# Kernel tuning notes

Measured on AMD Instinct MI355X. Metric: run time of the kernel, lower is better.

The kernel has to match this reference:

```python
import jax, jax.numpy as jnp
import numpy as np

N_NODES = 100000

def _graphconv(x, edge_src, edge_dst, norm_src, norm_dst, W, b):
    # DGL GraphConv with norm='both': D_out^{-1/2} A D_in^{-1/2} X W + b
    h = x * norm_src[:, None]                       # [N, d] src normalization
    msg = jnp.take(h, edge_src, axis=0)             # [E, d] gather
    agg = jax.ops.segment_sum(msg, edge_dst, num_segments=N_NODES)  # [N, d] scatter-add
    h = agg * norm_dst[:, None]                      # dst normalization
    return h @ W + b

def _degree_norms(edge_src, edge_dst):
    ones = jnp.ones(edge_src.shape[0], dtype=jnp.float32)
    deg_out = jax.ops.segment_sum(ones, edge_src, num_segments=N_NODES)
    deg_in = jax.ops.segment_sum(ones, edge_dst, num_segments=N_NODES)
    norm_src = jnp.where(deg_out > 0, jax.lax.rsqrt(jnp.maximum(deg_out, 1.0)), 0.0)
    norm_dst = jnp.where(deg_in > 0, jax.lax.rsqrt(jnp.maximum(deg_in, 1.0)), 0.0)
    return norm_src, norm_dst

def setup_inputs() -> dict:
    key = jax.random.key(0)
    ks = jax.random.split(key, 8)
    E = 1600000
    in_f, h_f, out_f = 128, 128, 64
    x = jax.random.normal(ks[0], (N_NODES, in_f), dtype=jnp.float32)
    edge_src = jax.random.randint(ks[1], (E,), 0, N_NODES, dtype=jnp.int32)
    edge_dst = jax.random.randint(ks[2], (E,), 0, N_NODES, dtype=jnp.int32)
    def glorot(k, shape):
        lim = np.sqrt(6.0 / (shape[0] + shape[1]))
        return jax.random.uniform(k, shape, jnp.float32, -lim, lim)
    W0 = glorot(ks[3], (in_f, h_f)); b0 = jnp.zeros((h_f,), jnp.float32)
    W1 = glorot(ks[4], (h_f, h_f)); b1 = jnp.zeros((h_f,), jnp.float32)
    W2 = glorot(ks[5], (h_f, out_f)); b2 = jnp.zeros((out_f,), jnp.float32)
    return {"x": x, "edge_src": edge_src, "edge_dst": edge_dst,
            "W0": W0, "b0": b0, "W1": W1, "b1": b1, "W2": W2, "b2": b2}

def reference(x, edge_src, edge_dst, W0, b0, W1, b1, W2, b2):
    norm_src, norm_dst = _degree_norms(edge_src, edge_dst)
    outputs = [x]
    h = jax.nn.relu(_graphconv(x, edge_src, edge_dst, norm_src, norm_dst, W0, b0))
    outputs.append(h)
    h = jax.nn.relu(_graphconv(h, edge_src, edge_dst, norm_src, norm_dst, W1, b1))
    outputs.append(h)
    h = _graphconv(h, edge_src, edge_dst, norm_src, norm_dst, W2, b2)
    outputs.append(h)
    return tuple(outputs)
```

## Files before the change

kernel.cpp:

```cpp
#include <hip/hip_runtime.h>

#define NN 100000
#define NE 1600000
#define NB 391
#define RS 32768
#define KR 4
#define RSL 64
#define SLICE 25000

typedef unsigned int uint;
typedef unsigned short ushort;
typedef unsigned char uchar;
typedef __attribute__((ext_vector_type(8))) short short8;
typedef __attribute__((ext_vector_type(4))) float f32x4;

__device__ __forceinline__ ushort f2bf(float f) {
    uint u = __float_as_uint(f);
    return (ushort)((u + 0x7FFFu + ((u >> 16) & 1u)) >> 16);
}

__device__ __forceinline__ void bf8_add(uint4 q, float* acc) {
    acc[0] += __uint_as_float(q.x << 16);
    acc[1] += __uint_as_float(q.x & 0xFFFF0000u);
    acc[2] += __uint_as_float(q.y << 16);
    acc[3] += __uint_as_float(q.y & 0xFFFF0000u);
    acc[4] += __uint_as_float(q.z << 16);
    acc[5] += __uint_as_float(q.z & 0xFFFF0000u);
    acc[6] += __uint_as_float(q.w << 16);
    acc[7] += __uint_as_float(q.w & 0xFFFF0000u);
}


__global__ __launch_bounds__(256)
void k_hist(const int* __restrict__ src, const int* __restrict__ dst,
            uchar* __restrict__ pout, uchar* __restrict__ pin) {
    int k = blockIdx.x >> 6, r = blockIdx.x & 63;
    __shared__ uint ho[RS / 4], hi[RS / 4];
    for (int i = threadIdx.x; i < RS / 4; i += 256) { ho[i] = 0; hi[i] = 0; }
    __syncthreads();
    int base = k * RS;
    int lo = r * SLICE, hiend = lo + SLICE;
    for (int i = lo + threadIdx.x; i < hiend; i += 256) {
        int s = src[i] - base;
        if ((uint)s < RS) atomicAdd(&ho[s >> 2], 1u << (8 * (s & 3)));
        int d = dst[i] - base;
        if ((uint)d < RS) atomicAdd(&hi[d >> 2], 1u << (8 * (d & 3)));
    }
    __syncthreads();
    uint* po = (uint*)(pout + ((size_t)k * RSL + r) * RS);
    uint* pi = (uint*)(pin + ((size_t)k * RSL + r) * RS);
    for (int i = threadIdx.x; i < RS / 4; i += 256) { po[i] = ho[i]; pi[i] = hi[i]; }
}


__global__ __launch_bounds__(256)
void k_red(const uchar* __restrict__ pout, uchar* __restrict__ pin,
           float* __restrict__ ns, float* __restrict__ nd,
           int* __restrict__ csum, int* __restrict__ bsum) {
    __shared__ int sred[256];
    int t = threadIdx.x;
    int n = blockIdx.x * 256 + t;
    int si = 0;
    if (n < NN) {
        int k = n >> 15, j = n & (RS - 1);
        const uchar* po = pout + (size_t)k * RSL * RS + j;
        uchar* pi = pin + (size_t)k * RSL * RS + j;
        int so = 0;
        #pragma unroll
        for (int r = 0; r < RSL; ++r) so += po[(size_t)r * RS];
        #pragma unroll
        for (int r = 0; r < RSL; ++r) {
            uchar c = pi[(size_t)r * RS];
            pi[(size_t)r * RS] = (uchar)si;
            si += c;
        }
        ns[n] = (so > 0) ? rsqrtf((float)so) : 0.f;
        nd[n] = (si > 0) ? rsqrtf((float)si) : 0.f;
        csum[n] = si;
    }
    sred[t] = si;
    __syncthreads();
    for (int off = 128; off > 0; off >>= 1) {
        if (t < off) sred[t] += sred[t + off];
        __syncthreads();
    }
    if (t == 0) bsum[blockIdx.x] = sred[0];
}


__global__ void k_scanb(const int* __restrict__ bsum, int* __restrict__ bsumex,
                        int* __restrict__ rowptr) {
    __shared__ int s[512];
    int t = threadIdx.x;
    int v = (t < NB) ? bsum[t] : 0;
    s[t] = v;
    __syncthreads();
    for (int off = 1; off < 512; off <<= 1) {
        int add = (t >= off) ? s[t - off] : 0;
        __syncthreads();
        s[t] += add;
        __syncthreads();
    }
    if (t < NB) bsumex[t] = s[t] - v;
    if (t == 0) rowptr[NN] = NE;
}

__global__ void k_rowptr(const int* __restrict__ cnt, const int* __restrict__ bsumex,
                         int* __restrict__ rowptr) {
    __shared__ int s[256];
    int t = threadIdx.x;
    int i = blockIdx.x * 256 + t;
    int v = (i < NN) ? cnt[i] : 0;
    s[t] = v;
    __syncthreads();
    for (int off = 1; off < 256; off <<= 1) {
        int add = (t >= off) ? s[t - off] : 0;
        __syncthreads();
        s[t] += add;
        __syncthreads();
    }
    if (i < NN) rowptr[i] = bsumex[blockIdx.x] + s[t] - v;
}


__global__ __launch_bounds__(256)
void k_fill(const int* __restrict__ src, const int* __restrict__ dst,
            const uchar* __restrict__ pin, const int* __restrict__ rowptr,
            int* __restrict__ csrc) {
    int k = blockIdx.x >> 6, r = blockIdx.x & 63;
    __shared__ uint cur[RS / 2];
    const uchar* pi = pin + ((size_t)k * RSL + r) * RS;
    for (int i = threadIdx.x; i < RS / 2; i += 256) {
        uint a = pi[2 * i], b = pi[2 * i + 1];
        cur[i] = a | (b << 16);
    }
    __syncthreads();
    int base = k * RS;
    int lo = r * SLICE, hiend = lo + SLICE;
    for (int i = lo + threadIdx.x; i < hiend; i += 256) {
        int d = dst[i];
        int j = d - base;
        if ((uint)j < RS) {
            uint old = atomicAdd(&cur[j >> 1], 1u << (16 * (j & 1)));
            int p = (old >> (16 * (j & 1))) & 0xFFFF;
            csrc[rowptr[d] + p] = src[i];
        }
    }
}


__global__ void k_wtall(const float* __restrict__ W0, const float* __restrict__ W1,
                        const float* __restrict__ W2, ushort* __restrict__ WT) {
    int i = blockIdx.x * 256 + threadIdx.x;
    if (i < 16384) {
        int n = i >> 7, k = i & 127;
        WT[i] = f2bf(W0[k * 128 + n]);
    } else if (i < 32768) {
        int j = i - 16384; int n = j >> 7, k = j & 127;
        WT[i] = f2bf(W1[k * 128 + n]);
    } else if (i < 40960) {
        int j = i - 32768; int n = j >> 7, k = j & 127;
        WT[i] = f2bf(W2[k * 64 + n]);
    }
}


__global__ void k_xcvt(const float4* __restrict__ x, float4* __restrict__ out,
                       ushort* __restrict__ xb, int n4) {
    int i = blockIdx.x * blockDim.x + threadIdx.x;
    if (i < n4) {
        float4 v = x[i];
        out[i] = v;
        ushort4 b;
        b.x = f2bf(v.x); b.y = f2bf(v.y); b.z = f2bf(v.z); b.w = f2bf(v.w);
        *(ushort4*)(xb + (size_t)i * 4) = b;
    }
}


template<int NT, int N>
__global__ __launch_bounds__(256)
void k_gemm_mfma(const ushort* __restrict__ Ab, const ushort* __restrict__ WT,
                 const float* __restrict__ ns, ushort* __restrict__ Cb) {
    int tid = threadIdx.x;
    int w = tid >> 6;
    int l = tid & 63;
    int li = l & 15;
    int kg = l >> 4;
    short8 bfrag[NT][4];
    #pragma unroll
    for (int n = 0; n < NT; ++n) {
        int col = w * 16 * NT + n * 16 + li;
        #pragma unroll
        for (int kt = 0; kt < 4; ++kt)
            bfrag[n][kt] = *(const short8*)(WT + (size_t)col * 128 + kt * 32 + kg * 8);
    }
    for (int mg = blockIdx.x; mg < NN / 16; mg += gridDim.x) {
        int row = mg * 16 + li;
        short8 afrag[4];
        #pragma unroll
        for (int kt = 0; kt < 4; ++kt)
            afrag[kt] = *(const short8*)(Ab + (size_t)row * 128 + kt * 32 + kg * 8);
        int crow = mg * 16 + kg * 4;
        float4 nsv = *(const float4*)(ns + crow);
        float nsa[4] = {nsv.x, nsv.y, nsv.z, nsv.w};
        #pragma unroll
        for (int n = 0; n < NT; ++n) {
            f32x4 acc = {0.f, 0.f, 0.f, 0.f};
            #pragma unroll
            for (int kt = 0; kt < 4; ++kt)
                acc = __builtin_amdgcn_mfma_f32_16x16x32_bf16(afrag[kt], bfrag[n][kt], acc, 0, 0, 0);
            int ccol = w * 16 * NT + n * 16 + li;
            #pragma unroll
            for (int r = 0; r < 4; ++r)
                Cb[(size_t)(crow + r) * N + ccol] = f2bf(acc[r] * nsa[r]);
        }
    }
}


template<bool RELU>
__global__ __launch_bounds__(256)
void k_agg128(const ushort* __restrict__ Yb, const int* __restrict__ rowptr,
              const int* __restrict__ csrc, const float* __restrict__ nd,
              const float* __restrict__ bias, float* __restrict__ out,
              ushort* __restrict__ outb) {
    int tid = threadIdx.x;
    int grp = tid >> 4;
    int lane = tid & 15;
    int node = blockIdx.x * 16 + grp;
    int beg = rowptr[node], end = rowptr[node + 1];
    float acc[8] = {0.f, 0.f, 0.f, 0.f, 0.f, 0.f, 0.f, 0.f};
    int e = beg;
    for (; e + 7 < end; e += 8) {
        int s0 = csrc[e];     int s1 = csrc[e + 1];
        int s2 = csrc[e + 2]; int s3 = csrc[e + 3];
        int s4 = csrc[e + 4]; int s5 = csrc[e + 5];
        int s6 = csrc[e + 6]; int s7 = csrc[e + 7];
        uint4 q0 = *(const uint4*)(Yb + (size_t)s0 * 128 + lane * 8);
        uint4 q1 = *(const uint4*)(Yb + (size_t)s1 * 128 + lane * 8);
        uint4 q2 = *(const uint4*)(Yb + (size_t)s2 * 128 + lane * 8);
        uint4 q3 = *(const uint4*)(Yb + (size_t)s3 * 128 + lane * 8);
        uint4 q4 = *(const uint4*)(Yb + (size_t)s4 * 128 + lane * 8);
        uint4 q5 = *(const uint4*)(Yb + (size_t)s5 * 128 + lane * 8);
        uint4 q6 = *(const uint4*)(Yb + (size_t)s6 * 128 + lane * 8);
        uint4 q7 = *(const uint4*)(Yb + (size_t)s7 * 128 + lane * 8);
        bf8_add(q0, acc); bf8_add(q1, acc); bf8_add(q2, acc); bf8_add(q3, acc);
        bf8_add(q4, acc); bf8_add(q5, acc); bf8_add(q6, acc); bf8_add(q7, acc);
    }
    for (; e + 3 < end; e += 4) {
        int s0 = csrc[e];     int s1 = csrc[e + 1];
        int s2 = csrc[e + 2]; int s3 = csrc[e + 3];
        uint4 q0 = *(const uint4*)(Yb + (size_t)s0 * 128 + lane * 8);
        uint4 q1 = *(const uint4*)(Yb + (size_t)s1 * 128 + lane * 8);
        uint4 q2 = *(const uint4*)(Yb + (size_t)s2 * 128 + lane * 8);
        uint4 q3 = *(const uint4*)(Yb + (size_t)s3 * 128 + lane * 8);
        bf8_add(q0, acc); bf8_add(q1, acc); bf8_add(q2, acc); bf8_add(q3, acc);
    }
    for (; e < end; ++e) {
        uint4 q = *(const uint4*)(Yb + (size_t)csrc[e] * 128 + lane * 8);
        bf8_add(q, acc);
    }
    float ndv = nd[node];
    float4 b0 = *(const float4*)(bias + lane * 8);
    float4 b1 = *(const float4*)(bias + lane * 8 + 4);
    float o[8];
    o[0] = acc[0] * ndv + b0.x; o[1] = acc[1] * ndv + b0.y;
    o[2] = acc[2] * ndv + b0.z; o[3] = acc[3] * ndv + b0.w;
    o[4] = acc[4] * ndv + b1.x; o[5] = acc[5] * ndv + b1.y;
    o[6] = acc[6] * ndv + b1.z; o[7] = acc[7] * ndv + b1.w;
    if (RELU) {
        #pragma unroll
        for (int i = 0; i < 8; ++i) o[i] = fmaxf(o[i], 0.f);
    }
    *(float4*)(out + (size_t)node * 128 + lane * 8)     = make_float4(o[0], o[1], o[2], o[3]);
    *(float4*)(out + (size_t)node * 128 + lane * 8 + 4) = make_float4(o[4], o[5], o[6], o[7]);
    short8 ob;
    #pragma unroll
    for (int i = 0; i < 8; ++i) ob[i] = (short)f2bf(o[i]);
    *(short8*)(outb + (size_t)node * 128 + lane * 8) = ob;
}

__global__ __launch_bounds__(256)
void k_agg64(const ushort* __restrict__ Yb, const int* __restrict__ rowptr,
             const int* __restrict__ csrc, const float* __restrict__ nd,
             const float* __restrict__ bias, float* __restrict__ out) {
    int tid = threadIdx.x;
    int grp = tid >> 3;
    int lane = tid & 7;
    int node = blockIdx.x * 32 + grp;
    int beg = rowptr[node], end = rowptr[node + 1];
    float acc[8] = {0.f, 0.f, 0.f, 0.f, 0.f, 0.f, 0.f, 0.f};
    int e = beg;
    for (; e + 7 < end; e += 8) {
        int s0 = csrc[e];     int s1 = csrc[e + 1];
        int s2 = csrc[e + 2]; int s3 = csrc[e + 3];
        int s4 = csrc[e + 4]; int s5 = csrc[e + 5];
        int s6 = csrc[e + 6]; int s7 = csrc[e + 7];
        uint4 q0 = *(const uint4*)(Yb + (size_t)s0 * 64 + lane * 8);
        uint4 q1 = *(const uint4*)(Yb + (size_t)s1 * 64 + lane * 8);
        uint4 q2 = *(const uint4*)(Yb + (size_t)s2 * 64 + lane * 8);
        uint4 q3 = *(const uint4*)(Yb + (size_t)s3 * 64 + lane * 8);
        uint4 q4 = *(const uint4*)(Yb + (size_t)s4 * 64 + lane * 8);
        uint4 q5 = *(const uint4*)(Yb + (size_t)s5 * 64 + lane * 8);
        uint4 q6 = *(const uint4*)(Yb + (size_t)s6 * 64 + lane * 8);
        uint4 q7 = *(const uint4*)(Yb + (size_t)s7 * 64 + lane * 8);
        bf8_add(q0, acc); bf8_add(q1, acc); bf8_add(q2, acc); bf8_add(q3, acc);
        bf8_add(q4, acc); bf8_add(q5, acc); bf8_add(q6, acc); bf8_add(q7, acc);
    }
    for (; e + 3 < end; e += 4) {
        int s0 = csrc[e];     int s1 = csrc[e + 1];
        int s2 = csrc[e + 2]; int s3 = csrc[e + 3];
        uint4 q0 = *(const uint4*)(Yb + (size_t)s0 * 64 + lane * 8);
        uint4 q1 = *(const uint4*)(Yb + (size_t)s1 * 64 + lane * 8);
        uint4 q2 = *(const uint4*)(Yb + (size_t)s2 * 64 + lane * 8);
        uint4 q3 = *(const uint4*)(Yb + (size_t)s3 * 64 + lane * 8);
        bf8_add(q0, acc); bf8_add(q1, acc); bf8_add(q2, acc); bf8_add(q3, acc);
    }
    for (; e < end; ++e) {
        uint4 q = *(const uint4*)(Yb + (size_t)csrc[e] * 64 + lane * 8);
        bf8_add(q, acc);
    }
    float ndv = nd[node];
    float4 b0 = *(const float4*)(bias + lane * 8);
    float4 b1 = *(const float4*)(bias + lane * 8 + 4);
    float4 o0, o1;
    o0.x = acc[0] * ndv + b0.x; o0.y = acc[1] * ndv + b0.y;
    o0.z = acc[2] * ndv + b0.z; o0.w = acc[3] * ndv + b0.w;
    o1.x = acc[4] * ndv + b1.x; o1.y = acc[5] * ndv + b1.y;
    o1.z = acc[6] * ndv + b1.z; o1.w = acc[7] * ndv + b1.w;
    *(float4*)(out + (size_t)node * 64 + lane * 8)     = o0;
    *(float4*)(out + (size_t)node * 64 + lane * 8 + 4) = o1;
}


extern "C" void kernel_launch(void* const* d_in, const int* in_sizes, int n_in,
                              void* d_out, int out_size, void* d_ws, size_t ws_size,
                              hipStream_t stream) {
    const float* x  = (const float*)d_in[0];
    const int* esrc = (const int*)d_in[1];
    const int* edst = (const int*)d_in[2];
    const float* W0 = (const float*)d_in[3];
    const float* b0 = (const float*)d_in[4];
    const float* W1 = (const float*)d_in[5];
    const float* b1 = (const float*)d_in[6];
    const float* W2 = (const float*)d_in[7];
    const float* b2 = (const float*)d_in[8];
    float* out = (float*)d_out;

    float* ns      = (float*)d_ws;
    float* nd      = ns + NN;
    int*   csum    = (int*)(nd + NN);
    int*   rowptr  = csum + NN;
    int*   bsum    = rowptr + NN + 8;
    int*   bsumex  = bsum + 512;
    int*   csrc    = bsumex + 512;
    uchar* pout    = (uchar*)(csrc + NE);
    uchar* pin     = pout + (size_t)KR * RSL * RS;
    ushort* WT0    = (ushort*)(pin + (size_t)KR * RSL * RS);
    ushort* WT1    = WT0 + 128 * 128;
    ushort* WT2    = WT1 + 128 * 128;
    ushort* Y2b    = WT2 + 64 * 128;
    ushort* xb     = Y2b + (size_t)NN * 64;
    ushort* h1b    = xb + (size_t)NN * 128;
    ushort* h2b    = h1b + (size_t)NN * 128;

    float* h1 = out + (size_t)NN * 128;
    float* h2 = h1 + (size_t)NN * 128;
    float* h3 = h2 + (size_t)NN * 128;

    ushort* Y0b = (ushort*)h2;
    ushort* Y1b = (ushort*)h3;

    k_hist<<<KR * RSL, 256, 0, stream>>>(esrc, edst, pout, pin);

    k_red<<<NB, 256, 0, stream>>>(pout, pin, ns, nd, csum, bsum);

    k_scanb<<<1, 512, 0, stream>>>(bsum, bsumex, rowptr);
    k_rowptr<<<NB, 256, 0, stream>>>(csum, bsumex, rowptr);

    k_fill<<<KR * RSL, 256, 0, stream>>>(esrc, edst, pin, rowptr, csrc);

    k_wtall<<<160, 256, 0, stream>>>(W0, W1, W2, WT0);

    k_xcvt<<<(NN * 32 + 255) / 256, 256, 0, stream>>>((const float4*)x, (float4*)out,
                                                      xb, NN * 32);

    k_gemm_mfma<2, 128><<<1024, 256, 0, stream>>>(xb, WT0, ns, Y0b);
    k_agg128<true><<<NN / 16, 256, 0, stream>>>(Y0b, rowptr, csrc, nd, b0, h1, h1b);

    k_gemm_mfma<2, 128><<<1024, 256, 0, stream>>>(h1b, WT1, ns, Y1b);
    k_agg128<true><<<NN / 16, 256, 0, stream>>>(Y1b, rowptr, csrc, nd, b1, h2, h2b);

    k_gemm_mfma<1, 64><<<1024, 256, 0, stream>>>(h2b, WT2, ns, Y2b);
    k_agg64<<<NN / 32, 256, 0, stream>>>(Y2b, rowptr, csrc, nd, b2, h3);
}
```

Measured before the change: 436.4 us.

## Fuse x conversion into first GEMM and fuse aggregation with next-layer GEMM

The separate fp32-to-bf16 conversion of x is folded into the first MFMA GEMM, which now reads fp32 x directly, converts it in registers and writes the copied output. Each 128-wide aggregation kernel now stages its bf16 result for 16 nodes in shared memory and immediately runs the next layer's MFMA projection, so the h1b/h2b bf16 intermediates and two GEMM launches disappear. This removes global round trips and launches, at the cost of per-block weight fragment reloads from global/L2 and a block-wide barrier inside the gather kernel.

```diff
diff --git a/kernel.cpp b/kernel.cpp
--- a/kernel.cpp
+++ b/kernel.cpp
@@ -165,32 +165,19 @@
 }
 
 
-__global__ void k_xcvt(const float4* __restrict__ x, float4* __restrict__ out,
-                       ushort* __restrict__ xb, int n4) {
-    int i = blockIdx.x * blockDim.x + threadIdx.x;
-    if (i < n4) {
-        float4 v = x[i];
-        out[i] = v;
-        ushort4 b;
-        b.x = f2bf(v.x); b.y = f2bf(v.y); b.z = f2bf(v.z); b.w = f2bf(v.w);
-        *(ushort4*)(xb + (size_t)i * 4) = b;
-    }
-}
-
-
-template<int NT, int N>
-__global__ __launch_bounds__(256)
-void k_gemm_mfma(const ushort* __restrict__ Ab, const ushort* __restrict__ WT,
-                 const float* __restrict__ ns, ushort* __restrict__ Cb) {
+__global__ __launch_bounds__(256)
+void k_gemm1(const float* __restrict__ A, const ushort* __restrict__ WT,
+             const float* __restrict__ ns, ushort* __restrict__ Cb,
+             float* __restrict__ xout) {
     int tid = threadIdx.x;
     int w = tid >> 6;
     int l = tid & 63;
     int li = l & 15;
     int kg = l >> 4;
-    short8 bfrag[NT][4];
+    short8 bfrag[2][4];
     #pragma unroll
-    for (int n = 0; n < NT; ++n) {
-        int col = w * 16 * NT + n * 16 + li;
+    for (int n = 0; n < 2; ++n) {
+        int col = w * 32 + n * 16 + li;
         #pragma unroll
         for (int kt = 0; kt < 4; ++kt)
             bfrag[n][kt] = *(const short8*)(WT + (size_t)col * 128 + kt * 32 + kg * 8);
@@ -199,36 +186,54 @@
         int row = mg * 16 + li;
         short8 afrag[4];
         #pragma unroll
-        for (int kt = 0; kt < 4; ++kt)
-            afrag[kt] = *(const short8*)(Ab + (size_t)row * 128 + kt * 32 + kg * 8);
+        for (int kt = 0; kt < 4; ++kt) {
+            const float* ap = A + (size_t)row * 128 + kt * 32 + kg * 8;
+            float4 a0 = *(const float4*)ap;
+            float4 a1 = *(const float4*)(ap + 4);
+            if (w == 0) {
+                float* op = xout + (size_t)row * 128 + kt * 32 + kg * 8;
+                *(float4*)op = a0;
+                *(float4*)(op + 4) = a1;
+            }
+            short8 af;
+            af[0] = (short)f2bf(a0.x); af[1] = (short)f2bf(a0.y);
+            af[2] = (short)f2bf(a0.z); af[3] = (short)f2bf(a0.w);
+            af[4] = (short)f2bf(a1.x); af[5] = (short)f2bf(a1.y);
+            af[6] = (short)f2bf(a1.z); af[7] = (short)f2bf(a1.w);
+            afrag[kt] = af;
+        }
         int crow = mg * 16 + kg * 4;
         float4 nsv = *(const float4*)(ns + crow);
         float nsa[4] = {nsv.x, nsv.y, nsv.z, nsv.w};
         #pragma unroll
-        for (int n = 0; n < NT; ++n) {
+        for (int n = 0; n < 2; ++n) {
             f32x4 acc = {0.f, 0.f, 0.f, 0.f};
             #pragma unroll
             for (int kt = 0; kt < 4; ++kt)
                 acc = __builtin_amdgcn_mfma_f32_16x16x32_bf16(afrag[kt], bfrag[n][kt], acc, 0, 0, 0);
-            int ccol = w * 16 * NT + n * 16 + li;
+            int ccol = w * 32 + n * 16 + li;
             #pragma unroll
             for (int r = 0; r < 4; ++r)
-                Cb[(size_t)(crow + r) * N + ccol] = f2bf(acc[r] * nsa[r]);
+                Cb[(size_t)(crow + r) * 128 + ccol] = f2bf(acc[r] * nsa[r]);
         }
     }
 }
 
 
-template<bool RELU>
-__global__ __launch_bounds__(256)
-void k_agg128(const ushort* __restrict__ Yb, const int* __restrict__ rowptr,
-              const int* __restrict__ csrc, const float* __restrict__ nd,
-              const float* __restrict__ bias, float* __restrict__ out,
-              ushort* __restrict__ outb) {
+template<int NOUT>
+__global__ __launch_bounds__(256)
+void k_agg_gemm(const ushort* __restrict__ Yb, const int* __restrict__ rowptr,
+                const int* __restrict__ csrc, const float* __restrict__ nd,
+                const float* __restrict__ bias, const float* __restrict__ ns,
+                const ushort* __restrict__ WT, float* __restrict__ hout,
+                ushort* __restrict__ Yout) {
+    constexpr int NT = NOUT / 64;
+    __shared__ ushort sA[16][136];
     int tid = threadIdx.x;
     int grp = tid >> 4;
     int lane = tid & 15;
-    int node = blockIdx.x * 16 + grp;
+    int node_base = blockIdx.x * 16;
+    int node = node_base + grp;
     int beg = rowptr[node], end = rowptr[node + 1];
     float acc[8] = {0.f, 0.f, 0.f, 0.f, 0.f, 0.f, 0.f, 0.f};
     int e = beg;
@@ -265,20 +270,43 @@
     float4 b0 = *(const float4*)(bias + lane * 8);
     float4 b1 = *(const float4*)(bias + lane * 8 + 4);
     float o[8];
-    o[0] = acc[0] * ndv + b0.x; o[1] = acc[1] * ndv + b0.y;
-    o[2] = acc[2] * ndv + b0.z; o[3] = acc[3] * ndv + b0.w;
-    o[4] = acc[4] * ndv + b1.x; o[5] = acc[5] * ndv + b1.y;
-    o[6] = acc[6] * ndv + b1.z; o[7] = acc[7] * ndv + b1.w;
-    if (RELU) {
-        #pragma unroll
-        for (int i = 0; i < 8; ++i) o[i] = fmaxf(o[i], 0.f);
-    }
-    *(float4*)(out + (size_t)node * 128 + lane * 8)     = make_float4(o[0], o[1], o[2], o[3]);
-    *(float4*)(out + (size_t)node * 128 + lane * 8 + 4) = make_float4(o[4], o[5], o[6], o[7]);
+    o[0] = fmaxf(acc[0] * ndv + b0.x, 0.f); o[1] = fmaxf(acc[1] * ndv + b0.y, 0.f);
+    o[2] = fmaxf(acc[2] * ndv + b0.z, 0.f); o[3] = fmaxf(acc[3] * ndv + b0.w, 0.f);
+    o[4] = fmaxf(acc[4] * ndv + b1.x, 0.f); o[5] = fmaxf(acc[5] * ndv + b1.y, 0.f);
+    o[6] = fmaxf(acc[6] * ndv + b1.z, 0.f); o[7] = fmaxf(acc[7] * ndv + b1.w, 0.f);
+    *(float4*)(hout + (size_t)node * 128 + lane * 8)     = make_float4(o[0], o[1], o[2], o[3]);
+    *(float4*)(hout + (size_t)node * 128 + lane * 8 + 4) = make_float4(o[4], o[5], o[6], o[7]);
     short8 ob;
     #pragma unroll
     for (int i = 0; i < 8; ++i) ob[i] = (short)f2bf(o[i]);
-    *(short8*)(outb + (size_t)node * 128 + lane * 8) = ob;
+    *(short8*)&sA[grp][lane * 8] = ob;
+    __syncthreads();
+
+    int w = tid >> 6;
+    int l = tid & 63;
+    int li = l & 15;
+    int kg = l >> 4;
+    short8 afrag[4];
+    #pragma unroll
+    for (int kt = 0; kt < 4; ++kt)
+        afrag[kt] = *(const short8*)&sA[li][kt * 32 + kg * 8];
+    float4 nsv = *(const float4*)(ns + node_base + kg * 4);
+    float nsa[4] = {nsv.x, nsv.y, nsv.z, nsv.w};
+    #pragma unroll
+    for (int n = 0; n < NT; ++n) {
+        int col = w * 16 * NT + n * 16 + li;
+        short8 bfrag[4];
+        #pragma unroll
+        for (int kt = 0; kt < 4; ++kt)
+            bfrag[kt] = *(const short8*)(WT + (size_t)col * 128 + kt * 32 + kg * 8);
+        f32x4 acc2 = {0.f, 0.f, 0.f, 0.f};
+        #pragma unroll
+        for (int kt = 0; kt < 4; ++kt)
+            acc2 = __builtin_amdgcn_mfma_f32_16x16x32_bf16(afrag[kt], bfrag[kt], acc2, 0, 0, 0);
+        #pragma unroll
+        for (int r = 0; r < 4; ++r)
+            Yout[(size_t)(node_base + kg * 4 + r) * NOUT + col] = f2bf(acc2[r] * nsa[r]);
+    }
 }
 
 __global__ __launch_bounds__(256)
@@ -361,9 +389,6 @@
     ushort* WT1    = WT0 + 128 * 128;
     ushort* WT2    = WT1 + 128 * 128;
     ushort* Y2b    = WT2 + 64 * 128;
-    ushort* xb     = Y2b + (size_t)NN * 64;
-    ushort* h1b    = xb + (size_t)NN * 128;
-    ushort* h2b    = h1b + (size_t)NN * 128;
 
     float* h1 = out + (size_t)NN * 128;
     float* h2 = h1 + (size_t)NN * 128;
@@ -383,15 +408,13 @@
 
     k_wtall<<<160, 256, 0, stream>>>(W0, W1, W2, WT0);
 
-    k_xcvt<<<(NN * 32 + 255) / 256, 256, 0, stream>>>((const float4*)x, (float4*)out,
-                                                      xb, NN * 32);
-
-    k_gemm_mfma<2, 128><<<1024, 256, 0, stream>>>(xb, WT0, ns, Y0b);
-    k_agg128<true><<<NN / 16, 256, 0, stream>>>(Y0b, rowptr, csrc, nd, b0, h1, h1b);
-
-    k_gemm_mfma<2, 128><<<1024, 256, 0, stream>>>(h1b, WT1, ns, Y1b);
-    k_agg128<true><<<NN / 16, 256, 0, stream>>>(Y1b, rowptr, csrc, nd, b1, h2, h2b);
-
-    k_gemm_mfma<1, 64><<<1024, 256, 0, stream>>>(h2b, WT2, ns, Y2b);
+    k_gemm1<<<1024, 256, 0, stream>>>(x, WT0, ns, Y0b, out);
+
+    k_agg_gemm<128><<<NN / 16, 256, 0, stream>>>(Y0b, rowptr, csrc, nd, b0, ns,
+                                                 WT1, h1, Y1b);
+
+    k_agg_gemm<64><<<NN / 16, 256, 0, stream>>>(Y1b, rowptr, csrc, nd, b1, ns,
+                                                WT2, h2, Y2b);
+
     k_agg64<<<NN / 32, 256, 0, stream>>>(Y2b, rowptr, csrc, nd, b2, h3);
 }
```

New measurement: 387.1 us, median of 2. -11.3%, faster.
